# Kernel optimization log

Hardware: AMD Instinct MI355X
Metric: run time of the kernel (lower is better)

The kernel has to match this reference:

```python
import jax, jax.numpy as jnp
import numpy as np

B, N, C = 16, 576, 1024
H, HD = 16, 64          # num_heads, head_dim
LMAX = 1024             # KV cache capacity
CUR = 256               # pre-existing cur_kv_len
HID = 4096              # mlp hidden
PREFIX = 64             # fixed prefix length from source
EPS = 1e-5


def _ln(x, w, b):
    m = x.mean(-1, keepdims=True)
    v = ((x - m) ** 2).mean(-1, keepdims=True)
    return (x - m) * jax.lax.rsqrt(v + EPS) * w + b


def setup_inputs() -> dict:
    key = jax.random.key(0)
    ks = jax.random.split(key, 8)
    s = 0.02
    return {
        "x": jax.random.normal(ks[0], (B, N, C), jnp.float32),
        "cache_k": jax.random.normal(ks[1], (B, H, LMAX, HD), jnp.float32),
        "cache_v": jax.random.normal(ks[2], (B, H, LMAX, HD), jnp.float32),
        "qkv_w": jax.random.normal(ks[3], (C, 3 * C), jnp.float32) * s,
        "qkv_b": jnp.zeros((3 * C,), jnp.float32),
        "proj_w": jax.random.normal(ks[4], (C, C), jnp.float32) * s,
        "proj_b": jnp.zeros((C,), jnp.float32),
        "norm1_w": jnp.ones((C,), jnp.float32),
        "norm1_b": jnp.zeros((C,), jnp.float32),
        "norm2_w": jnp.ones((C,), jnp.float32),
        "norm2_b": jnp.zeros((C,), jnp.float32),
        "fc1_w": jax.random.normal(ks[5], (C, HID), jnp.float32) * s,
        "fc1_b": jnp.zeros((HID,), jnp.float32),
        "fc2_w": jax.random.normal(ks[6], (HID, C), jnp.float32) * s,
        "fc2_b": jnp.zeros((C,), jnp.float32),
        "cur_kv_len": CUR,
    }


def reference(x, cache_k, cache_v, qkv_w, qkv_b, proj_w, proj_b,
              norm1_w, norm1_b, norm2_w, norm2_b,
              fc1_w, fc1_b, fc2_w, fc2_b, cur_kv_len):
    b, n, c = x.shape
    hd = c // H
    scale = hd ** -0.5

    # ---- attention branch (lazy_mar, not force-fresh) ----
    h = _ln(x, norm1_w, norm1_b)
    qkv = (h @ qkv_w + qkv_b).reshape(b, n, 3, H, hd).transpose(2, 0, 3, 1, 4)
    q, k, v = qkv[0], qkv[1], qkv[2]          # [B,H,N,hd]

    L = cur_kv_len                            # python int -> static slices
    app = n - PREFIX
    # scatter new keys/values into the cache: prefix at [0:64], lazy region appended
    ck = cache_k.at[:, :, PREFIX + L:PREFIX + L + app, :].set(k[:, :, PREFIX:, :])
    ck = ck.at[:, :, :PREFIX, :].set(k[:, :, :PREFIX, :])
    cv = cache_v.at[:, :, PREFIX + L:PREFIX + L + app, :].set(v[:, :, PREFIX:, :])
    cv = cv.at[:, :, :PREFIX, :].set(v[:, :, :PREFIX, :])

    avail = L + n                             # (L + app) + 64
    attn = jax.nn.softmax(
        jnp.einsum('bhqd,bhkd->bhqk', q * scale, ck[:, :, :avail, :]), axis=-1)
    o = jnp.einsum('bhqk,bhkd->bhqd', attn, cv[:, :, :avail, :])
    o = o.transpose(0, 2, 1, 3).reshape(b, n, c)
    x = x + (o @ proj_w + proj_b)

    # ---- MLP branch ----
    h2 = _ln(x, norm2_w, norm2_b)
    mlp = jax.nn.gelu(h2 @ fc1_w + fc1_b, approximate=False) @ fc2_w + fc2_b
    return x + mlp
```

## Files before the change

kernel.cpp:

```cpp
#include <hip/hip_runtime.h>

#define Bb 16
#define Nn_ 576
#define Cc 1024
#define Hh 16
#define HD 64
#define HID 4096
#define AVAIL 832
#define ROWS (Bb*Nn_)

typedef __bf16 bf16x8 __attribute__((ext_vector_type(8)));
typedef float f32x4 __attribute__((ext_vector_type(4)));

__device__ __forceinline__ unsigned short f2bf(float f) {
  unsigned u = __float_as_uint(f);
  u += 0x7FFF + ((u >> 16) & 1);
  return (unsigned short)(u >> 16);
}

__device__ __forceinline__ void glds16(const void* g, void* l) {
  __builtin_amdgcn_global_load_lds(
      (const __attribute__((address_space(1))) void*)g,
      (__attribute__((address_space(3))) void*)l, 16, 0, 0);
}

__device__ __forceinline__ bf16x8 ds_read128(const void* p) {
  bf16x8 r;
  asm volatile("ds_read_b128 %0, %1"
               : "=v"(r)
               : "v"((const __attribute__((address_space(3))) char*)p));
  return r;
}

#define BARR() asm volatile("s_barrier" ::: "memory")
#define VMCNT8() asm volatile("s_waitcnt vmcnt(8)" ::: "memory")
#define VMCNT0() asm volatile("s_waitcnt vmcnt(0)" ::: "memory")
#define LGKM0() asm volatile("s_waitcnt lgkmcnt(0)" ::: "memory")
#define SCHEDB() __builtin_amdgcn_sched_barrier(0)

__global__ void wtrans2_k(const float* __restrict__ in, unsigned short* __restrict__ out,
                          int K, int N) {
  __shared__ float tile[64][65];
  int k0 = blockIdx.x * 64, n0 = blockIdx.y * 64;
  int tid = threadIdx.x;
  int nl = tid & 63, kl0 = tid >> 6;
#pragma unroll
  for (int j = 0; j < 16; j++) {
    int kl = kl0 + j * 4;
    tile[nl][kl] = in[(size_t)(k0 + kl) * N + n0 + nl];
  }
  __syncthreads();
  int no0 = tid >> 3, ko = (tid & 7) * 8;
#pragma unroll
  for (int i = 0; i < 2; i++) {
    int no = no0 + i * 32;
    const float* tp = &tile[no][ko];
    ushort4 oa, ob;
    oa.x = f2bf(tp[0]); oa.y = f2bf(tp[1]); oa.z = f2bf(tp[2]); oa.w = f2bf(tp[3]);
    ob.x = f2bf(tp[4]); ob.y = f2bf(tp[5]); ob.z = f2bf(tp[6]); ob.w = f2bf(tp[7]);
    unsigned short* op = &out[(size_t)(n0 + no) * K + k0 + ko];
    *(ushort4*)op = oa;
    *(ushort4*)(op + 4) = ob;
  }
}

__global__ void ln_k(const float* __restrict__ x, const float* __restrict__ w,
                     const float* __restrict__ bi, unsigned short* __restrict__ out) {
  int row = blockIdx.x;
  int t = threadIdx.x;
  float4 v = ((const float4*)(x + (size_t)row * Cc))[t];
  float s = v.x + v.y + v.z + v.w;
  float s2 = v.x * v.x + v.y * v.y + v.z * v.z + v.w * v.w;
#pragma unroll
  for (int off = 1; off < 64; off <<= 1) { s += __shfl_xor(s, off); s2 += __shfl_xor(s2, off); }
  __shared__ float red[8];
  int wid = t >> 6, lane = t & 63;
  if (lane == 0) { red[wid] = s; red[4 + wid] = s2; }
  __syncthreads();
  s = red[0] + red[1] + red[2] + red[3];
  s2 = red[4] + red[5] + red[6] + red[7];
  float mean = s * (1.0f / Cc);
  float var = s2 * (1.0f / Cc) - mean * mean;
  float rstd = rsqrtf(var + 1e-5f);
  float4 wv = ((const float4*)w)[t];
  float4 bv = ((const float4*)bi)[t];
  ushort4 ov;
  ov.x = f2bf((v.x - mean) * rstd * wv.x + bv.x);
  ov.y = f2bf((v.y - mean) * rstd * wv.y + bv.y);
  ov.z = f2bf((v.z - mean) * rstd * wv.z + bv.z);
  ov.w = f2bf((v.w - mean) * rstd * wv.w + bv.w);
  *(ushort4*)(out + (size_t)row * Cc + t * 4) = ov;
}

template <int EPI>
__global__ __launch_bounds__(256, 2) void gemmD_k(
    const unsigned short* __restrict__ A, const unsigned short* __restrict__ Bt,
    const float* __restrict__ bias, const float* __restrict__ resid,
    void* __restrict__ outv, int N, int K) {
  extern __shared__ __align__(16) char smem[];
  char* A0buf = smem;
  char* B0buf = smem + 16384;
  char* A1buf = smem + 32768;
  char* B1buf = smem + 49152;

  const int tid = threadIdx.x, lane = tid & 63, wid = tid >> 6;
  const int wr = wid >> 1, wc = wid & 1;
  const int l15 = lane & 15, l4 = lane >> 4;
  const int m0 = blockIdx.x * 128, n0 = blockIdx.y * 128;
  const int KT = K >> 6;
  const size_t K2 = (size_t)K * 2;

  const int toff = (tid >> 3) * (int)K2 + ((((tid & 7) ^ ((tid >> 3) & 7)) << 4));
  const char* AsD = (const char*)A + (size_t)m0 * K2 + toff;
  const char* BsD = (const char*)Bt + (size_t)n0 * K2 + toff;
  const size_t l32 = 32 * K2;
  const int dst = tid * 16;

  const int s0 = ((l4 ^ (l15 & 7)) << 4);
  const int rbA = (wr * 64 + l15) * 128;
  const int rbB = (wc * 64 + l15) * 128;

  f32x4 acc[4][4] = {};
  bf16x8 av[4][2], bv[4][2];

#define DSTAGE(src, ktb, ldsT)                  \
  do {                                          \
    const char* _g = (src) + (size_t)(ktb);     \
    glds16(_g, (ldsT) + dst);                   \
    glds16(_g + l32, (ldsT) + 4096 + dst);      \
    glds16(_g + 2 * l32, (ldsT) + 8192 + dst);  \
    glds16(_g + 3 * l32, (ldsT) + 12288 + dst); \
  } while (0)

#define DRD(CA, CB)                                                          \
  do {                                                                       \
    _Pragma("unroll") for (int mi = 0; mi < 4; ++mi)                         \
    _Pragma("unroll") for (int ks = 0; ks < 2; ++ks)                         \
      av[mi][ks] = ds_read128((CA) + rbA + mi * 2048 + (s0 ^ (ks << 6)));    \
    _Pragma("unroll") for (int ni = 0; ni < 4; ++ni)                         \
    _Pragma("unroll") for (int ks = 0; ks < 2; ++ks)                         \
      bv[ni][ks] = ds_read128((CB) + rbB + ni * 2048 + (s0 ^ (ks << 6)));    \
  } while (0)

#define DMF()                                                                \
  _Pragma("unroll") for (int mi = 0; mi < 4; ++mi)                           \
  _Pragma("unroll") for (int ni = 0; ni < 4; ++ni)                           \
  _Pragma("unroll") for (int ks = 0; ks < 2; ++ks)                           \
    acc[mi][ni] = __builtin_amdgcn_mfma_f32_16x16x32_bf16(                   \
        av[mi][ks], bv[ni][ks], acc[mi][ni], 0, 0, 0);

  DSTAGE(AsD, 0, A0buf);
  DSTAGE(BsD, 0, B0buf);
  DSTAGE(AsD, 128, A1buf);
  DSTAGE(BsD, 128, B1buf);
  VMCNT8();
  BARR();

#pragma unroll 1
  for (int t = 0; t + 3 < KT; t += 2) {
    DRD(A0buf, B0buf);
    LGKM0(); SCHEDB(); BARR();
    DSTAGE(AsD, (size_t)(t + 2) * 128, A0buf);
    DSTAGE(BsD, (size_t)(t + 2) * 128, B0buf);
    __builtin_amdgcn_s_setprio(1); DMF(); __builtin_amdgcn_s_setprio(0);
    VMCNT8(); BARR();
    DRD(A1buf, B1buf);
    LGKM0(); SCHEDB(); BARR();
    DSTAGE(AsD, (size_t)(t + 3) * 128, A1buf);
    DSTAGE(BsD, (size_t)(t + 3) * 128, B1buf);
    __builtin_amdgcn_s_setprio(1); DMF(); __builtin_amdgcn_s_setprio(0);
    VMCNT8(); BARR();
  }
  DRD(A0buf, B0buf);
  LGKM0(); SCHEDB(); BARR();
  __builtin_amdgcn_s_setprio(1); DMF(); __builtin_amdgcn_s_setprio(0);
  VMCNT0(); BARR();
  DRD(A1buf, B1buf);
  LGKM0(); SCHEDB();
  DMF();

  BARR();
  {
    float* eb = (float*)(smem + wid * 8192);
    const int gc0 = n0 + wc * 64;
    const f32x4 bv4 = *(const f32x4*)&bias[gc0 + l15 * 4];
#pragma unroll
    for (int mi = 0; mi < 4; mi++) {
#pragma unroll
      for (int ni = 0; ni < 4; ni++)
#pragma unroll
        for (int j = 0; j < 4; j++)
          eb[(l4 * 4 + j) * 68 + ni * 16 + l15] = acc[mi][ni][j];
      int gr0 = m0 + wr * 64 + mi * 16;
#pragma unroll
      for (int k = 0; k < 4; k++) {
        int r = k * 4 + l4;
        f32x4 v = *(const f32x4*)&eb[r * 68 + l15 * 4];
        v += bv4;
        size_t base = (size_t)(gr0 + r) * N + gc0 + l15 * 4;
        if (EPI == 1) {
#pragma unroll
          for (int q = 0; q < 4; q++)
            v[q] = 0.5f * v[q] * (1.0f + erff(v[q] * 0.70710678118f));
        }
        if (EPI == 2) {
          f32x4 rv = *(const f32x4*)&resid[base];
          *(f32x4*)((float*)outv + base) = v + rv;
        } else {
          ushort4 o4;
          o4.x = f2bf(v[0]); o4.y = f2bf(v[1]); o4.z = f2bf(v[2]); o4.w = f2bf(v[3]);
          *(ushort4*)((unsigned short*)outv + base) = o4;
        }
      }
    }
  }
#undef DMF
#undef DRD
#undef DSTAGE
}

__global__ void gatherk_k(const unsigned short* __restrict__ qkv,
                          const float* __restrict__ cache_k,
                          unsigned short* __restrict__ Kg) {
  int bh = blockIdx.y, b = bh >> 4, h = bh & 15;
  int p = blockIdx.x * 4 + (threadIdx.x >> 6);
  int d = threadIdx.x & 63;
  unsigned short val;
  if (p < 64)
    val = qkv[((size_t)(b * Nn_ + p)) * 3072 + 1024 + h * 64 + d];
  else if (p < 320)
    val = f2bf(cache_k[(((size_t)b * Hh + h) * 1024 + p) * 64 + d]);
  else
    val = qkv[((size_t)(b * Nn_ + p - 256)) * 3072 + 1024 + h * 64 + d];
  Kg[(((size_t)bh) * AVAIL + p) * 64 + d] = val;
}

__global__ void gathervt_k(const unsigned short* __restrict__ qkv,
                           const float* __restrict__ cache_v,
                           unsigned short* __restrict__ Vt) {
  __shared__ float tile[32][33];
  int bh = blockIdx.z, b = bh >> 4, h = bh & 15;
  int p0 = blockIdx.x * 32, d0 = blockIdx.y * 32;
  int tx = threadIdx.x, ty = threadIdx.y;
#pragma unroll
  for (int i = 0; i < 4; i++) {
    int p = p0 + ty + i * 8, d = d0 + tx;
    float v;
    if (p < 64)
      v = __uint_as_float((unsigned)qkv[((size_t)(b * Nn_ + p)) * 3072 + 2048 + h * 64 + d] << 16);
    else if (p < 320)
      v = cache_v[(((size_t)b * Hh + h) * 1024 + p) * 64 + d];
    else
      v = __uint_as_float((unsigned)qkv[((size_t)(b * Nn_ + p - 256)) * 3072 + 2048 + h * 64 + d] << 16);
    tile[ty + i * 8][tx] = v;
  }
  __syncthreads();
#pragma unroll
  for (int i = 0; i < 4; i++)
    Vt[(((size_t)bh) * 64 + d0 + ty + i * 8) * AVAIL + p0 + tx] = f2bf(tile[tx][ty + i * 8]);
}

__global__ __launch_bounds__(256) void attn_k(
    const unsigned short* __restrict__ qkv, const unsigned short* __restrict__ Kg,
    const unsigned short* __restrict__ Vt, unsigned short* __restrict__ o) {
  __shared__ __attribute__((aligned(16))) unsigned short Qs[64 * 64];
  __shared__ __attribute__((aligned(16))) unsigned short Ks[2][64 * 64];
  __shared__ __attribute__((aligned(16))) unsigned short Vs[2][64 * 64];
  __shared__ __attribute__((aligned(16))) unsigned short Ps[4][16 * 64];

  const int tid = threadIdx.x;
  const int lane = tid & 63;
  const int w = tid >> 6;
  const int qt = blockIdx.x;
  const int bh = blockIdx.y, b = bh >> 4, h = bh & 15;
  const float scale = 0.125f;

  const char* kbase = (const char*)(Kg + (size_t)bh * AVAIL * 64);
  const char* vbase = (const char*)(Vt + (size_t)bh * 64 * AVAIL);
  const int vr = tid >> 3;
  const int vcb = (tid & 7) << 4;

#define STAGE_KV(c, buf)                                                          \
  do {                                                                            \
    glds16(kbase + (size_t)(c) * 8192 + tid * 16, (char*)Ks[buf] + tid * 16);     \
    glds16(kbase + (size_t)(c) * 8192 + 4096 + tid * 16,                          \
           (char*)Ks[buf] + 4096 + tid * 16);                                     \
    glds16(vbase + (size_t)vr * (AVAIL * 2) + (c) * 128 + vcb,                    \
           (char*)Vs[buf] + tid * 16);                                            \
    glds16(vbase + (size_t)(vr + 32) * (AVAIL * 2) + (c) * 128 + vcb,             \
           (char*)Vs[buf] + 4096 + tid * 16);                                     \
  } while (0)

  {
    const char* qb = (const char*)qkv;
    glds16(qb + ((size_t)(b * Nn_ + qt * 64 + vr) * 3072 + h * 64) * 2 + vcb,
           (char*)Qs + tid * 16);
    glds16(qb + ((size_t)(b * Nn_ + qt * 64 + 32 + vr) * 3072 + h * 64) * 2 + vcb,
           (char*)Qs + 4096 + tid * 16);
  }
  STAGE_KV(0, 0);
  asm volatile("s_waitcnt vmcnt(0)" ::: "memory");
  __syncthreads();

  bf16x8 qf[2];
#pragma unroll
  for (int t = 0; t < 2; t++)
    qf[t] = *(const bf16x8*)&Qs[(w * 16 + (lane & 15)) * 64 + t * 32 + (lane >> 4) * 8];

  float m_run[4], l_run[4];
  f32x4 oacc[4] = {};
#pragma unroll
  for (int j = 0; j < 4; j++) { m_run[j] = -1e30f; l_run[j] = 0.f; }

  for (int c = 0; c < 13; c++) {
    const int cur = c & 1;
    if (c < 12) STAGE_KV(c + 1, cur ^ 1);

    f32x4 s[4] = {};
#pragma unroll
    for (int nt = 0; nt < 4; nt++) {
#pragma unroll
      for (int t = 0; t < 2; t++) {
        bf16x8 kf =
            *(const bf16x8*)&Ks[cur][(nt * 16 + (lane & 15)) * 64 + t * 32 + (lane >> 4) * 8];
        s[nt] = __builtin_amdgcn_mfma_f32_16x16x32_bf16(qf[t], kf, s[nt], 0, 0, 0);
      }
    }

    float p[4][4];
#pragma unroll
    for (int j = 0; j < 4; j++) {
      float mx = fmaxf(fmaxf(s[0][j], s[1][j]), fmaxf(s[2][j], s[3][j])) * scale;
#pragma unroll
      for (int off = 1; off < 16; off <<= 1) mx = fmaxf(mx, __shfl_xor(mx, off));
      float m_new = fmaxf(m_run[j], mx);
      float alpha = __expf(m_run[j] - m_new);
      float sum = 0.f;
#pragma unroll
      for (int nt = 0; nt < 4; nt++) {
        p[nt][j] = __expf(s[nt][j] * scale - m_new);
        sum += p[nt][j];
      }
#pragma unroll
      for (int off = 1; off < 16; off <<= 1) sum += __shfl_xor(sum, off);
      l_run[j] = l_run[j] * alpha + sum;
      m_run[j] = m_new;
#pragma unroll
      for (int nt2 = 0; nt2 < 4; nt2++) oacc[nt2][j] *= alpha;
    }

#pragma unroll
    for (int nt = 0; nt < 4; nt++)
#pragma unroll
      for (int j = 0; j < 4; j++)
        Ps[w][((lane >> 4) * 4 + j) * 64 + nt * 16 + (lane & 15)] = f2bf(p[nt][j]);

    bf16x8 pa[2];
#pragma unroll
    for (int t = 0; t < 2; t++)
      pa[t] = *(const bf16x8*)&Ps[w][(lane & 15) * 64 + t * 32 + (lane >> 4) * 8];
#pragma unroll
    for (int nt2 = 0; nt2 < 4; nt2++) {
#pragma unroll
      for (int t = 0; t < 2; t++) {
        bf16x8 vf =
            *(const bf16x8*)&Vs[cur][(nt2 * 16 + (lane & 15)) * 64 + t * 32 + (lane >> 4) * 8];
        oacc[nt2] = __builtin_amdgcn_mfma_f32_16x16x32_bf16(pa[t], vf, oacc[nt2], 0, 0, 0);
      }
    }
    __syncthreads();
  }

#pragma unroll
  for (int nt2 = 0; nt2 < 4; nt2++) {
#pragma unroll
    for (int j = 0; j < 4; j++) {
      int q = qt * 64 + w * 16 + (lane >> 4) * 4 + j;
      float v = oacc[nt2][j] / l_run[j];
      o[((size_t)(b * Nn_ + q)) * Cc + h * 64 + nt2 * 16 + (lane & 15)] = f2bf(v);
    }
  }
#undef STAGE_KV
}

extern "C" void kernel_launch(void* const* d_in, const int* in_sizes, int n_in,
                              void* d_out, int out_size, void* d_ws, size_t ws_size,
                              hipStream_t stream) {
  const float* x = (const float*)d_in[0];
  const float* cache_k = (const float*)d_in[1];
  const float* cache_v = (const float*)d_in[2];
  const float* qkv_w = (const float*)d_in[3];
  const float* qkv_b = (const float*)d_in[4];
  const float* proj_w = (const float*)d_in[5];
  const float* proj_b = (const float*)d_in[6];
  const float* n1w = (const float*)d_in[7];
  const float* n1b = (const float*)d_in[8];
  const float* n2w = (const float*)d_in[9];
  const float* n2b = (const float*)d_in[10];
  const float* fc1w = (const float*)d_in[11];
  const float* fc1b = (const float*)d_in[12];
  const float* fc2w = (const float*)d_in[13];
  const float* fc2b = (const float*)d_in[14];

  char* ws = (char*)d_ws;
  unsigned short* wq_t = (unsigned short*)(ws + 0);
  unsigned short* wp_t = (unsigned short*)(ws + 6291456);
  unsigned short* w1_t = (unsigned short*)(ws + 8388608);
  unsigned short* w2_t = (unsigned short*)(ws + 16777216);
  float* x2           = (float*)(ws + 25165824);
  unsigned short* obuf = (unsigned short*)(ws + 62914560);
  unsigned short* hbuf = (unsigned short*)(ws + 81788928);
  unsigned short* vt   = (unsigned short*)(ws + 100663296);
  unsigned short* qkvb = (unsigned short*)(ws + 127926272);
  unsigned short* kg   = (unsigned short*)(ws + 184549376);
  unsigned short* midb = qkvb;

  hipFuncSetAttribute((const void*)&gemmD_k<0>, hipFuncAttributeMaxDynamicSharedMemorySize, 65536);
  hipFuncSetAttribute((const void*)&gemmD_k<1>, hipFuncAttributeMaxDynamicSharedMemorySize, 65536);
  hipFuncSetAttribute((const void*)&gemmD_k<2>, hipFuncAttributeMaxDynamicSharedMemorySize, 65536);

  wtrans2_k<<<dim3(16, 48), 256, 0, stream>>>(qkv_w, wq_t, 1024, 3072);
  wtrans2_k<<<dim3(16, 16), 256, 0, stream>>>(proj_w, wp_t, 1024, 1024);
  wtrans2_k<<<dim3(16, 64), 256, 0, stream>>>(fc1w, w1_t, 1024, 4096);
  wtrans2_k<<<dim3(64, 16), 256, 0, stream>>>(fc2w, w2_t, 4096, 1024);

  ln_k<<<ROWS, 256, 0, stream>>>(x, n1w, n1b, hbuf);
  gemmD_k<0><<<dim3(72, 24), 256, 65536, stream>>>(hbuf, wq_t, qkv_b, nullptr, qkvb, 3072, 1024);

  gatherk_k<<<dim3(208, 256), 256, 0, stream>>>(qkvb, cache_k, kg);
  gathervt_k<<<dim3(26, 2, 256), dim3(32, 8), 0, stream>>>(qkvb, cache_v, vt);
  attn_k<<<dim3(9, 256), 256, 0, stream>>>(qkvb, kg, vt, obuf);

  gemmD_k<2><<<dim3(72, 8), 256, 65536, stream>>>(obuf, wp_t, proj_b, x, x2, 1024, 1024);
  ln_k<<<ROWS, 256, 0, stream>>>(x2, n2w, n2b, hbuf);

  gemmD_k<1><<<dim3(72, 32), 256, 65536, stream>>>(hbuf, w1_t, fc1b, nullptr, midb, 4096, 1024);
  gemmD_k<2><<<dim3(72, 8), 256, 65536, stream>>>(midb, w2_t, fc2b, x2, (float*)d_out, 1024, 4096);
}
```

Before: 529.8 us.

## Replace double-buffered GEMM with single-buffer BK=32 kernel at higher occupancy

```diff
diff --git a/kernel.cpp b/kernel.cpp
--- a/kernel.cpp
+++ b/kernel.cpp
@@ -24,19 +24,7 @@
       (__attribute__((address_space(3))) void*)l, 16, 0, 0);
 }
 
-__device__ __forceinline__ bf16x8 ds_read128(const void* p) {
-  bf16x8 r;
-  asm volatile("ds_read_b128 %0, %1"
-               : "=v"(r)
-               : "v"((const __attribute__((address_space(3))) char*)p));
-  return r;
-}
-
-#define BARR() asm volatile("s_barrier" ::: "memory")
-#define VMCNT8() asm volatile("s_waitcnt vmcnt(8)" ::: "memory")
 #define VMCNT0() asm volatile("s_waitcnt vmcnt(0)" ::: "memory")
-#define LGKM0() asm volatile("s_waitcnt lgkmcnt(0)" ::: "memory")
-#define SCHEDB() __builtin_amdgcn_sched_barrier(0)
 
 __global__ void wtrans2_k(const float* __restrict__ in, unsigned short* __restrict__ out,
                           int K, int N) {
@@ -93,95 +81,63 @@
 }
 
 template <int EPI>
-__global__ __launch_bounds__(256, 2) void gemmD_k(
+__global__ __launch_bounds__(256, 4) void gemmE_k(
     const unsigned short* __restrict__ A, const unsigned short* __restrict__ Bt,
     const float* __restrict__ bias, const float* __restrict__ resid,
     void* __restrict__ outv, int N, int K) {
   extern __shared__ __align__(16) char smem[];
-  char* A0buf = smem;
-  char* B0buf = smem + 16384;
-  char* A1buf = smem + 32768;
-  char* B1buf = smem + 49152;
+  char* Abuf = smem;
+  char* Bbuf = smem + 8192;
 
   const int tid = threadIdx.x, lane = tid & 63, wid = tid >> 6;
   const int wr = wid >> 1, wc = wid & 1;
   const int l15 = lane & 15, l4 = lane >> 4;
   const int m0 = blockIdx.x * 128, n0 = blockIdx.y * 128;
-  const int KT = K >> 6;
+  const int KT = K >> 5;
   const size_t K2 = (size_t)K * 2;
 
-  const int toff = (tid >> 3) * (int)K2 + ((((tid & 7) ^ ((tid >> 3) & 7)) << 4));
+  const int toff = (tid >> 2) * (int)K2 + ((((tid & 3) ^ ((tid >> 2) & 3)) << 4));
   const char* AsD = (const char*)A + (size_t)m0 * K2 + toff;
   const char* BsD = (const char*)Bt + (size_t)n0 * K2 + toff;
-  const size_t l32 = 32 * K2;
+  const size_t l64h = 64 * K2;
   const int dst = tid * 16;
 
-  const int s0 = ((l4 ^ (l15 & 7)) << 4);
-  const int rbA = (wr * 64 + l15) * 128;
-  const int rbB = (wc * 64 + l15) * 128;
+  const int sw = ((l4 ^ (l15 & 3)) << 4);
+  const int rbA = (wr * 64 + l15) * 64;
+  const int rbB = (wc * 64 + l15) * 64;
 
   f32x4 acc[4][4] = {};
-  bf16x8 av[4][2], bv[4][2];
-
-#define DSTAGE(src, ktb, ldsT)                  \
-  do {                                          \
-    const char* _g = (src) + (size_t)(ktb);     \
-    glds16(_g, (ldsT) + dst);                   \
-    glds16(_g + l32, (ldsT) + 4096 + dst);      \
-    glds16(_g + 2 * l32, (ldsT) + 8192 + dst);  \
-    glds16(_g + 3 * l32, (ldsT) + 12288 + dst); \
-  } while (0)
-
-#define DRD(CA, CB)                                                          \
-  do {                                                                       \
-    _Pragma("unroll") for (int mi = 0; mi < 4; ++mi)                         \
-    _Pragma("unroll") for (int ks = 0; ks < 2; ++ks)                         \
-      av[mi][ks] = ds_read128((CA) + rbA + mi * 2048 + (s0 ^ (ks << 6)));    \
-    _Pragma("unroll") for (int ni = 0; ni < 4; ++ni)                         \
-    _Pragma("unroll") for (int ks = 0; ks < 2; ++ks)                         \
-      bv[ni][ks] = ds_read128((CB) + rbB + ni * 2048 + (s0 ^ (ks << 6)));    \
-  } while (0)
-
-#define DMF()                                                                \
-  _Pragma("unroll") for (int mi = 0; mi < 4; ++mi)                           \
-  _Pragma("unroll") for (int ni = 0; ni < 4; ++ni)                           \
-  _Pragma("unroll") for (int ks = 0; ks < 2; ++ks)                           \
-    acc[mi][ni] = __builtin_amdgcn_mfma_f32_16x16x32_bf16(                   \
-        av[mi][ks], bv[ni][ks], acc[mi][ni], 0, 0, 0);
-
-  DSTAGE(AsD, 0, A0buf);
-  DSTAGE(BsD, 0, B0buf);
-  DSTAGE(AsD, 128, A1buf);
-  DSTAGE(BsD, 128, B1buf);
-  VMCNT8();
-  BARR();
 
 #pragma unroll 1
-  for (int t = 0; t + 3 < KT; t += 2) {
-    DRD(A0buf, B0buf);
-    LGKM0(); SCHEDB(); BARR();
-    DSTAGE(AsD, (size_t)(t + 2) * 128, A0buf);
-    DSTAGE(BsD, (size_t)(t + 2) * 128, B0buf);
-    __builtin_amdgcn_s_setprio(1); DMF(); __builtin_amdgcn_s_setprio(0);
-    VMCNT8(); BARR();
-    DRD(A1buf, B1buf);
-    LGKM0(); SCHEDB(); BARR();
-    DSTAGE(AsD, (size_t)(t + 3) * 128, A1buf);
-    DSTAGE(BsD, (size_t)(t + 3) * 128, B1buf);
-    __builtin_amdgcn_s_setprio(1); DMF(); __builtin_amdgcn_s_setprio(0);
-    VMCNT8(); BARR();
-  }
-  DRD(A0buf, B0buf);
-  LGKM0(); SCHEDB(); BARR();
-  __builtin_amdgcn_s_setprio(1); DMF(); __builtin_amdgcn_s_setprio(0);
-  VMCNT0(); BARR();
-  DRD(A1buf, B1buf);
-  LGKM0(); SCHEDB();
-  DMF();
-
-  BARR();
+  for (int t = 0; t < KT; ++t) {
+    const size_t kb = (size_t)t * 64;
+    glds16(AsD + kb, Abuf + dst);
+    glds16(AsD + kb + l64h, Abuf + 4096 + dst);
+    glds16(BsD + kb, Bbuf + dst);
+    glds16(BsD + kb + l64h, Bbuf + 4096 + dst);
+    VMCNT0();
+    __syncthreads();
+
+    bf16x8 av[4], bv[4];
+#pragma unroll
+    for (int mi = 0; mi < 4; ++mi)
+      av[mi] = *(const bf16x8*)(Abuf + rbA + mi * 1024 + sw);
+#pragma unroll
+    for (int ni = 0; ni < 4; ++ni)
+      bv[ni] = *(const bf16x8*)(Bbuf + rbB + ni * 1024 + sw);
+    __builtin_amdgcn_s_setprio(1);
+#pragma unroll
+    for (int mi = 0; mi < 4; ++mi)
+#pragma unroll
+      for (int ni = 0; ni < 4; ++ni)
+        acc[mi][ni] = __builtin_amdgcn_mfma_f32_16x16x32_bf16(av[mi], bv[ni], acc[mi][ni], 0, 0, 0);
+    __builtin_amdgcn_s_setprio(0);
+    __syncthreads();
+  }
+
+  __syncthreads();
   {
-    float* eb = (float*)(smem + wid * 8192);
+    float* eb = (float*)(smem + wid * 4096);
     const int gc0 = n0 + wc * 64;
     const f32x4 bv4 = *(const f32x4*)&bias[gc0 + l15 * 4];
 #pragma unroll
@@ -190,12 +146,13 @@
       for (int ni = 0; ni < 4; ni++)
 #pragma unroll
         for (int j = 0; j < 4; j++)
-          eb[(l4 * 4 + j) * 68 + ni * 16 + l15] = acc[mi][ni][j];
+          eb[(l4 * 4 + j) * 64 + ni * 16 + l15] = acc[mi][ni][j];
+      __builtin_amdgcn_s_waitcnt(0);
       int gr0 = m0 + wr * 64 + mi * 16;
 #pragma unroll
       for (int k = 0; k < 4; k++) {
         int r = k * 4 + l4;
-        f32x4 v = *(const f32x4*)&eb[r * 68 + l15 * 4];
+        f32x4 v = *(const f32x4*)&eb[r * 64 + l15 * 4];
         v += bv4;
         size_t base = (size_t)(gr0 + r) * N + gc0 + l15 * 4;
         if (EPI == 1) {
@@ -214,9 +171,6 @@
       }
     }
   }
-#undef DMF
-#undef DRD
-#undef DSTAGE
 }
 
 __global__ void gatherk_k(const unsigned short* __restrict__ qkv,
@@ -299,7 +253,7 @@
            (char*)Qs + 4096 + tid * 16);
   }
   STAGE_KV(0, 0);
-  asm volatile("s_waitcnt vmcnt(0)" ::: "memory");
+  VMCNT0();
   __syncthreads();
 
   bf16x8 qf[2];
@@ -415,9 +369,9 @@
   unsigned short* kg   = (unsigned short*)(ws + 184549376);
   unsigned short* midb = qkvb;
 
-  hipFuncSetAttribute((const void*)&gemmD_k<0>, hipFuncAttributeMaxDynamicSharedMemorySize, 65536);
-  hipFuncSetAttribute((const void*)&gemmD_k<1>, hipFuncAttributeMaxDynamicSharedMemorySize, 65536);
-  hipFuncSetAttribute((const void*)&gemmD_k<2>, hipFuncAttributeMaxDynamicSharedMemorySize, 65536);
+  hipFuncSetAttribute((const void*)&gemmE_k<0>, hipFuncAttributeMaxDynamicSharedMemorySize, 16384);
+  hipFuncSetAttribute((const void*)&gemmE_k<1>, hipFuncAttributeMaxDynamicSharedMemorySize, 16384);
+  hipFuncSetAttribute((const void*)&gemmE_k<2>, hipFuncAttributeMaxDynamicSharedMemorySize, 16384);
 
   wtrans2_k<<<dim3(16, 48), 256, 0, stream>>>(qkv_w, wq_t, 1024, 3072);
   wtrans2_k<<<dim3(16, 16), 256, 0, stream>>>(proj_w, wp_t, 1024, 1024);
@@ -425,15 +379,15 @@
   wtrans2_k<<<dim3(64, 16), 256, 0, stream>>>(fc2w, w2_t, 4096, 1024);
 
   ln_k<<<ROWS, 256, 0, stream>>>(x, n1w, n1b, hbuf);
-  gemmD_k<0><<<dim3(72, 24), 256, 65536, stream>>>(hbuf, wq_t, qkv_b, nullptr, qkvb, 3072, 1024);
+  gemmE_k<0><<<dim3(72, 24), 256, 16384, stream>>>(hbuf, wq_t, qkv_b, nullptr, qkvb, 3072, 1024);
 
   gatherk_k<<<dim3(208, 256), 256, 0, stream>>>(qkvb, cache_k, kg);
   gathervt_k<<<dim3(26, 2, 256), dim3(32, 8), 0, stream>>>(qkvb, cache_v, vt);
   attn_k<<<dim3(9, 256), 256, 0, stream>>>(qkvb, kg, vt, obuf);
 
-  gemmD_k<2><<<dim3(72, 8), 256, 65536, stream>>>(obuf, wp_t, proj_b, x, x2, 1024, 1024);
+  gemmE_k<2><<<dim3(72, 8), 256, 16384, stream>>>(obuf, wp_t, proj_b, x, x2, 1024, 1024);
   ln_k<<<ROWS, 256, 0, stream>>>(x2, n2w, n2b, hbuf);
 
-  gemmD_k<1><<<dim3(72, 32), 256, 65536, stream>>>(hbuf, w1_t, fc1b, nullptr, midb, 4096, 1024);
-  gemmD_k<2><<<dim3(72, 8), 256, 65536, stream>>>(midb, w2_t, fc2b, x2, (float*)d_out, 1024, 4096);
-}
+  gemmE_k<1><<<dim3(72, 32), 256, 16384, stream>>>(hbuf, w1_t, fc1b, nullptr, midb, 4096, 1024);
+  gemmE_k<2><<<dim3(72, 8), 256, 16384, stream>>>(midb, w2_t, fc2b, x2, (float*)d_out, 1024, 4096);
+}
```

Result: slower. 565.2 us (+6.7%).
